# Kernel tuning notes

Measured on AMD Instinct MI355X. Metric: run time of the kernel, lower is better.

Reference implementation:

```python
import jax, jax.numpy as jnp
import numpy as np

B, F, D = 4096, 39, 16          # batch, num_field, embedding_size
V = 1000000                     # num_feat (vocab)
H1, H2 = 128, 128               # cin_layer_sizes
INPUT_DIM = F * D               # 624
FC_DIM = H1 // 2 + H2           # 192 (split_half)
DEEP = [400, 400]
BN_EPS = 1e-5


def setup_inputs() -> dict:
    key = jax.random.key(0)
    ks = jax.random.split(key, 16)
    xav = lambda k, shp: jax.random.normal(k, shp, jnp.float32) * np.sqrt(2.0 / (shp[0] + shp[-1]))
    return {
        "feat_index": jax.random.randint(ks[0], (B, F), 0, V),
        "feat_value": jax.random.uniform(ks[1], (B, F), jnp.float32),
        "emb_table": xav(ks[2], (V, D)),
        "linear_w": xav(ks[3], (INPUT_DIM, 1)),
        "linear_b": jnp.zeros((1,), jnp.float32),
        "conv_w1": xav(ks[4], (H1, F, F)),          # (out, h_prev, m) == conv1d 1x1 weight reshaped
        "conv_b1": jnp.zeros((H1,), jnp.float32),
        "conv_w2": xav(ks[5], (H2, H1 // 2, F)),
        "conv_b2": jnp.zeros((H2,), jnp.float32),
        "deep_w1": xav(ks[6], (INPUT_DIM, DEEP[0])),
        "deep_b1": jnp.zeros((DEEP[0],), jnp.float32),
        "bn_g1": jnp.ones((DEEP[0],), jnp.float32),
        "bn_b1": jnp.zeros((DEEP[0],), jnp.float32),
        "deep_w2": xav(ks[7], (DEEP[0], DEEP[1])),
        "deep_b2": jnp.zeros((DEEP[1],), jnp.float32),
        "bn_g2": jnp.ones((DEEP[1],), jnp.float32),
        "bn_b2": jnpp if False else jnp.zeros((DEEP[1],), jnp.float32),
        "out_w": xav(ks[8], (1 + FC_DIM + DEEP[1], 1)),
        "out_b": jnp.zeros((1,), jnp.float32),
    }


def _bn(x, g, b):
    # torch BatchNorm1d in training mode: biased batch variance
    m = x.mean(axis=0)
    v = x.var(axis=0)
    return g * (x - m) * jax.lax.rsqrt(v + BN_EPS) + b


def reference(feat_index, feat_value, emb_table, linear_w, linear_b,
              conv_w1, conv_b1, conv_w2, conv_b2,
              deep_w1, deep_b1, bn_g1, bn_b1,
              deep_w2, deep_b2, bn_g2, bn_b2,
              out_w, out_b):
    e = emb_table[feat_index]                      # [B, F, D]
    flat = e.reshape(e.shape[0], -1)               # [B, F*D]
    linear_part = flat @ linear_w + linear_b       # [B, 1]

    # CIN: fused outer-product + 1x1 conv (x_k[b,o,d] = sum_{h,m} W[o,h,m] x_prev[b,h,d] x0[b,m,d])
    x0 = e
    h1 = jax.nn.relu(jnp.einsum('bhd,bmd,ohm->bod', x0, x0, conv_w1) + conv_b1[None, :, None])
    nxt, hi1 = jnp.split(h1, 2, axis=1)            # split_half
    h2 = jax.nn.relu(jnp.einsum('bhd,bmd,ohm->bod', nxt, x0, conv_w2) + conv_b2[None, :, None])
    res = jnp.concatenate([hi1, h2], axis=1).sum(axis=2)   # [B, FC_DIM]

    # Deep tower (dropout off / deterministic)
    y = jax.nn.relu(_bn(flat @ deep_w1 + deep_b1, bn_g1, bn_b1))
    y = jax.nn.relu(_bn(y @ deep_w2 + deep_b2, bn_g2, bn_b2))

    cat = jnp.concatenate([linear_part, res, y], axis=1)   # [B, 593]
    return cat @ out_w + out_b
```

## Files before the change

kernel.cpp:

```cpp
#include <hip/hip_runtime.h>

#define BATCH   4096
#define NF      39
#define ED      16
#define IN_DIM  624
#define DW      400
#define BN_EPS  1e-5f
#define NK16    156
#define AK1     640
#define NKS1    20
#define NKS2    13
#define WCOL    416

typedef __attribute__((ext_vector_type(8))) short short8;
typedef __attribute__((ext_vector_type(16))) float f32x16;
typedef __attribute__((ext_vector_type(4))) float f32x4;
typedef __attribute__((ext_vector_type(2))) float f32x2;
typedef unsigned short u16;

__device__ inline unsigned pack_hi2(float a, float b) {
  return __builtin_amdgcn_perm(__float_as_uint(b), __float_as_uint(a), 0x07060302u);
}
__device__ inline unsigned bf16_rne(float f) {
  unsigned u = __float_as_uint(f);
  u += 0x7fff + ((u >> 16) & 1);
  return u >> 16;
}
__device__ inline float bf2f(u16 v) { return __uint_as_float((unsigned)v << 16); }

#define CIN_E (NK16 * 128 * 16)
#define D1_E  (NKS1 * WCOL * 32)
#define D2_E  (NKS2 * WCOL * 32)
#define PREP_E (CIN_E + D1_E + D2_E + 1600)
#define PREP_B ((PREP_E + 255) / 256)
#define GATH_B (BATCH / 4)

__global__ __launch_bounds__(256) void k_gp(const int* __restrict__ idx,
    const float* __restrict__ emb, const float* __restrict__ lw,
    const float* __restrict__ lb, const float* __restrict__ w1,
    const float* __restrict__ w2, const float* __restrict__ dw1,
    const float* __restrict__ dw2, u16* __restrict__ flatb,
    float* __restrict__ lp, u16* __restrict__ wp1, u16* __restrict__ wp2,
    u16* __restrict__ wpd1, u16* __restrict__ wpd2, float* __restrict__ gstat) {
  int t = threadIdx.x;
  if (blockIdx.x < GATH_B) {
    int lane = t & 63;
    int b = blockIdx.x * 4 + (t >> 6);
    int sj = (lane < NF) ? idx[b * NF + lane] : 0;
    float acc = 0.f;
#pragma unroll
    for (int i = 0; i < 10; i++) {
      int e = lane + i * 64;
      if (e < IN_DIM) {
        int f = e >> 4;
        int row = __shfl(sj, f);
        float v = emb[(size_t)row * ED + (e & 15)];
        flatb[(size_t)b * AK1 + e] = (u16)bf16_rne(v);
        acc = fmaf(v, lw[e], acc);
      } else {
        flatb[(size_t)b * AK1 + e] = 0;
      }
    }
#pragma unroll
    for (int k = 1; k < 64; k <<= 1) acc += __shfl_xor(acc, k);
    if (lane == 0) lp[b] = acc + lb[0];
  } else {
    int e = (blockIdx.x - GATH_B) * 256 + t;
    if (e < CIN_E) {
      int k16 = e >> 11, r = e & 2047, col = r >> 4, kk = r & 15;
      int k = k16 * 16 + kk, h = k & 63, m = k >> 6;
      float v1 = (h < NF) ? w1[(size_t)col * (NF * NF) + h * NF + m] : 0.f;
      float v2 = w2[(size_t)col * (64 * NF) + h * NF + m];
      wp1[e] = (u16)bf16_rne(v1);
      wp2[e] = (u16)bf16_rne(v2);
    } else if (e < CIN_E + D1_E) {
      int e2 = e - CIN_E;
      int ksg = e2 / (WCOL * 32), r = e2 - ksg * (WCOL * 32);
      int col = r >> 5, kk = r & 31;
      int k = ksg * 32 + kk;
      wpd1[e2] = (k < IN_DIM && col < DW) ? (u16)bf16_rne(dw1[(size_t)k * DW + col]) : 0;
    } else if (e < CIN_E + D1_E + D2_E) {
      int e2 = e - CIN_E - D1_E;
      int ksg = e2 / (WCOL * 32), r = e2 - ksg * (WCOL * 32);
      int col = r >> 5, kk = r & 31;
      int k = ksg * 32 + kk;
      wpd2[e2] = (k < DW && col < DW) ? (u16)bf16_rne(dw2[(size_t)k * DW + col]) : 0;
    } else if (e < PREP_E) {
      gstat[e - CIN_E - D1_E - D2_E] = 0.f;
    }
  }
}

template <bool LAY2>
__global__ __launch_bounds__(256, 2) void k_cin32(
    const u16* __restrict__ flatb, const u16* __restrict__ nxtg,
    const u16* __restrict__ wp, const float* __restrict__ bias,
    u16* __restrict__ nxt_out, float* __restrict__ res) {
  int t = threadIdx.x;
  int w = t >> 6, lane = t & 63;
  int col = lane & 31, khalf = lane >> 5;
  int si = (lane >> 4) & 1, d = lane & 15;
  int b0 = blockIdx.x * 8 + w * 2;
  int b = b0 + si;
  const u16* fb = flatb + (size_t)b * AK1;

  f32x2 sp[4][4];
  if (LAY2) {
#pragma unroll
    for (int s = 0; s < 4; s++) {
      uint4 v = *(const uint4*)(nxtg + (((size_t)b * 16 + d) * 64 + s * 16 + khalf * 8));
      unsigned uu[4] = {v.x, v.y, v.z, v.w};
#pragma unroll
      for (int w4 = 0; w4 < 4; w4++)
        sp[s][w4] = (f32x2){__uint_as_float(uu[w4] << 16),
                            __uint_as_float(uu[w4] & 0xffff0000u)};
    }
  } else {
#pragma unroll
    for (int s = 0; s < 4; s++)
#pragma unroll
      for (int w4 = 0; w4 < 4; w4++) {
        int h0 = s * 16 + khalf * 8 + 2 * w4;
        int h1 = h0 + 1;
        float f0 = (h0 < NF) ? bf2f(fb[h0 * 16 + d]) : 0.f;
        float f1 = (h1 < NF) ? bf2f(fb[h1 * 16 + d]) : 0.f;
        sp[s][w4] = (f32x2){f0, f1};
      }
  }

  f32x16 acc[4];
#pragma unroll
  for (int nt = 0; nt < 4; nt++)
#pragma unroll
    for (int r = 0; r < 16; r++) acc[nt][r] = 0.f;

  const u16* wbase = wp + (size_t)col * 16 + khalf * 8;
  short8 bfr[3][4];
#pragma unroll
  for (int nt = 0; nt < 4; nt++) {
    bfr[0][nt] = *(const short8*)(wbase + nt * 512);
    bfr[1][nt] = *(const short8*)(wbase + 2048 + nt * 512);
  }

  float xv = bf2f(fb[d]);
  float xvn;

  for (int mg = 0; mg < 13; mg++) {
#pragma unroll
    for (int j = 0; j < 12; j++) {
      int k16 = mg * 12 + j;
      if (j == 0 || j == 4 || j == 8) {
        int mn = mg * 3 + (j >> 2) + 1;
        xvn = bf2f(fb[mn * 16 + d]);
      }
      if (j < 10 || mg < 12) {
        const u16* wb = wbase + (size_t)(k16 + 2) * 2048;
#pragma unroll
        for (int nt = 0; nt < 4; nt++)
          bfr[(j + 2) % 3][nt] = *(const short8*)(wb + nt * 512);
      }
      int s = j & 3;
      union { unsigned u[4]; short8 v; } a;
      f32x2 xv2 = (f32x2){xv, xv};
#pragma unroll
      for (int w4 = 0; w4 < 4; w4++) {
        f32x2 p = sp[s][w4] * xv2;
        a.u[w4] = pack_hi2(p[0], p[1]);
      }
#pragma unroll
      for (int nt = 0; nt < 4; nt++)
        acc[nt] = __builtin_amdgcn_mfma_f32_32x32x16_bf16(
            a.v, bfr[j % 3][nt], acc[nt], 0, 0, 0);
      if (s == 3) xv = xvn;
    }
  }

#pragma unroll
  for (int nt = 0; nt < 4; nt++) {
    int o = nt * 32 + col;
    float bi = bias[o];
    if (!LAY2 && nt < 2) {
#pragma unroll
      for (int r = 0; r < 16; r++) {
        int si2 = r >> 3;
        int dd = (r & 3) + 8 * ((r >> 2) & 1) + 4 * khalf;
        float v = fmaxf(acc[nt][r] + bi, 0.f);
        nxt_out[((size_t)(b0 + si2) * 16 + dd) * 64 + o] = (u16)bf16_rne(v);
      }
    } else {
      float p0 = 0.f, p1 = 0.f;
#pragma unroll
      for (int r = 0; r < 8; r++)  p0 += fmaxf(acc[nt][r] + bi, 0.f);
#pragma unroll
      for (int r = 8; r < 16; r++) p1 += fmaxf(acc[nt][r] + bi, 0.f);
      p0 += __shfl_xor(p0, 32);
      p1 += __shfl_xor(p1, 32);
      if (khalf == 0) {
        int ri = LAY2 ? (64 + o) : (o - 64);
        res[(size_t)b0 * 192 + ri] = p0;
        res[(size_t)(b0 + 1) * 192 + ri] = p1;
      }
    }
  }
}

template <bool BN_A, int NKS, int KREAL, int AK>
__global__ __launch_bounds__(256) void k_gemm_mfma(
    const u16* __restrict__ Abf, const float* __restrict__ Af32,
    const u16* __restrict__ wp, const float* __restrict__ bias,
    const float* __restrict__ gsIn, const float* __restrict__ gs2In,
    const float* __restrict__ bng, const float* __restrict__ bnb,
    float* __restrict__ C, float* __restrict__ gs, float* __restrict__ gs2) {
  __shared__ float lsS[NKS * 32], lsH[NKS * 32];
  __shared__ float lred[64];
  int t = threadIdx.x;
  if (BN_A) {
    for (int c = t; c < NKS * 32; c += 256) {
      float sc = 0.f, sh = 0.f;
      if (c < DW) {
        float m = gsIn[c] * (1.f / BATCH);
        float var = gs2In[c] * (1.f / BATCH) - m * m;
        sc = bng[c] * rsqrtf(var + BN_EPS);
        sh = bnb[c] - m * sc;
      }
      lsS[c] = sc; lsH[c] = sh;
    }
  }
  if (t < 64) lred[t] = 0.f;
  __syncthreads();

  int w = t >> 6, lane = t & 63;
  int nl = lane & 15, q = lane >> 4;
  int row = blockIdx.x * 64 + w * 16 + nl;
  int c0 = blockIdx.y * 32;
  f32x4 acc[2];
  acc[0] = (f32x4){0.f, 0.f, 0.f, 0.f};
  acc[1] = (f32x4){0.f, 0.f, 0.f, 0.f};

  short8 araw[2]; f32x4 fraw0[2], fraw1[2]; short8 braw[2][2];
  auto loadA_raw = [&](int ksg, int buf) {
    int kb = ksg * 32 + q * 8;
    if (!BN_A) {
      araw[buf] = *(const short8*)(Abf + (size_t)row * AK + kb);
    } else {
      if (kb + 8 <= KREAL) {
        fraw0[buf] = *(const f32x4*)(Af32 + (size_t)row * KREAL + kb);
        fraw1[buf] = *(const f32x4*)(Af32 + (size_t)row * KREAL + kb + 4);
      } else {
        fraw0[buf] = (f32x4){0.f,0.f,0.f,0.f};
        fraw1[buf] = (f32x4){0.f,0.f,0.f,0.f};
      }
    }
    const u16* wb = wp + (size_t)ksg * (WCOL * 32) + (size_t)(c0 + nl) * 32 + q * 8;
    braw[buf][0] = *(const short8*)wb;
    braw[buf][1] = *(const short8*)(wb + 16 * 32);
  };
  auto cookA = [&](int ksg, int buf) -> short8 {
    if (!BN_A) return araw[buf];
    int kb = ksg * 32 + q * 8;
    f32x4 s0 = *(const f32x4*)&lsS[kb], h0 = *(const f32x4*)&lsH[kb];
    f32x4 s1 = *(const f32x4*)&lsS[kb + 4], h1 = *(const f32x4*)&lsH[kb + 4];
    union { unsigned u[4]; short8 s; } a;
    float v0 = fmaxf(fmaf(fraw0[buf][0], s0[0], h0[0]), 0.f);
    float v1 = fmaxf(fmaf(fraw0[buf][1], s0[1], h0[1]), 0.f);
    float v2 = fmaxf(fmaf(fraw0[buf][2], s0[2], h0[2]), 0.f);
    float v3 = fmaxf(fmaf(fraw0[buf][3], s0[3], h0[3]), 0.f);
    float v4 = fmaxf(fmaf(fraw1[buf][0], s1[0], h1[0]), 0.f);
    float v5 = fmaxf(fmaf(fraw1[buf][1], s1[1], h1[1]), 0.f);
    float v6 = fmaxf(fmaf(fraw1[buf][2], s1[2], h1[2]), 0.f);
    float v7 = fmaxf(fmaf(fraw1[buf][3], s1[3], h1[3]), 0.f);
    a.u[0] = bf16_rne(v0) | (bf16_rne(v1) << 16);
    a.u[1] = bf16_rne(v2) | (bf16_rne(v3) << 16);
    a.u[2] = bf16_rne(v4) | (bf16_rne(v5) << 16);
    a.u[3] = bf16_rne(v6) | (bf16_rne(v7) << 16);
    return a.s;
  };

  loadA_raw(0, 0);
#pragma unroll 4
  for (int ksg = 0; ksg < NKS; ksg++) {
    int cur = ksg & 1;
    if (ksg + 1 < NKS) loadA_raw(ksg + 1, cur ^ 1);
    short8 afr = cookA(ksg, cur);
    acc[0] = __builtin_amdgcn_mfma_f32_16x16x32_bf16(afr, braw[cur][0], acc[0], 0, 0, 0);
    acc[1] = __builtin_amdgcn_mfma_f32_16x16x32_bf16(afr, braw[cur][1], acc[1], 0, 0, 0);
  }

  int rbase = blockIdx.x * 64 + w * 16 + q * 4;
#pragma unroll
  for (int nt = 0; nt < 2; nt++) {
    int col = c0 + nt * 16 + nl;
    if (col < DW) {
      float bi = bias[col];
      float s = 0.f, s2 = 0.f;
#pragma unroll
      for (int r = 0; r < 4; r++) {
        float v = acc[nt][r] + bi;
        C[(size_t)(rbase + r) * DW + col] = v;
        s += v; s2 = fmaf(v, v, s2);
      }
      s += __shfl_xor(s, 16); s2 += __shfl_xor(s2, 16);
      s += __shfl_xor(s, 32); s2 += __shfl_xor(s2, 32);
      if (q == 0) {
        atomicAdd(&lred[nt * 16 + nl], s);
        atomicAdd(&lred[32 + nt * 16 + nl], s2);
      }
    }
  }
  __syncthreads();
  if (t < 32) {
    int col = c0 + t;
    if (col < DW) atomicAdd(&gs[col], lred[t]);
  } else if (t < 64) {
    int col = c0 + t - 32;
    if (col < DW) atomicAdd(&gs2[col], lred[t]);
  }
}

__global__ __launch_bounds__(256) void k_final(const float* __restrict__ lp,
    const float* __restrict__ res, const float* __restrict__ y2,
    const float* __restrict__ gB, const float* __restrict__ gB2,
    const float* __restrict__ g2, const float* __restrict__ bb2,
    const float* __restrict__ ow, const float* __restrict__ ob,
    float* __restrict__ out) {
  __shared__ float lsS[DW], lsH[DW];
  int t = threadIdx.x;
  for (int c = t; c < DW; c += 256) {
    float m = gB[c] * (1.f / BATCH);
    float var = gB2[c] * (1.f / BATCH) - m * m;
    float sc = g2[c] * rsqrtf(var + BN_EPS);
    lsS[c] = sc;
    lsH[c] = bb2[c] - m * sc;
  }
  __syncthreads();
  int lane = t & 63, w = t >> 6;
  int b = blockIdx.x * 4 + w;
  float acc = 0.f;
  for (int j = lane; j < 593; j += 64) {
    float v;
    if (j == 0)       v = lp[b];
    else if (j < 193) v = res[(size_t)b * 192 + (j - 1)];
    else {
      int c = j - 193;
      v = fmaxf(fmaf(y2[(size_t)b * DW + c], lsS[c], lsH[c]), 0.f);
    }
    acc = fmaf(v, ow[j], acc);
  }
#pragma unroll
  for (int k = 1; k < 64; k <<= 1) acc += __shfl_xor(acc, k);
  if (lane == 0) out[b] = acc + ob[0];
}

extern "C" void kernel_launch(void* const* d_in, const int* in_sizes, int n_in,
                              void* d_out, int out_size, void* d_ws, size_t ws_size,
                              hipStream_t stream) {
  const int*   feat_index = (const int*)d_in[0];
  const float* emb = (const float*)d_in[2];
  const float* lw  = (const float*)d_in[3];
  const float* lb  = (const float*)d_in[4];
  const float* w1  = (const float*)d_in[5];
  const float* b1  = (const float*)d_in[6];
  const float* w2  = (const float*)d_in[7];
  const float* b2  = (const float*)d_in[8];
  const float* dw1 = (const float*)d_in[9];
  const float* db1 = (const float*)d_in[10];
  const float* g1  = (const float*)d_in[11];
  const float* bb1 = (const float*)d_in[12];
  const float* dw2 = (const float*)d_in[13];
  const float* db2 = (const float*)d_in[14];
  const float* g2  = (const float*)d_in[15];
  const float* bb2 = (const float*)d_in[16];
  const float* ow  = (const float*)d_in[17];
  const float* ob  = (const float*)d_in[18];

  float* ws   = (float*)d_ws;
  u16*  flatb = (u16*)ws;
  float* y1   = ws + 1310720;
  float* res  = ws + 2949120;
  float* lp   = ws + 3735552;
  float* gA   = ws + 3741248;
  float* gA2  = gA + 400;
  float* gB   = gA2 + 400;
  float* gB2  = gB + 400;
  u16*  nxtg  = (u16*)(ws + 3742848);
  float* y2   = ws + 3742848;
  u16*  wp1   = (u16*)(ws + 5840000);
  u16*  wp2   = (u16*)(ws + 5999744);
  u16*  wpd1  = (u16*)(ws + 6159488);
  u16*  wpd2  = (u16*)(ws + 6292608);
  float* out  = (float*)d_out;

  k_gp<<<GATH_B + PREP_B, 256, 0, stream>>>(feat_index, emb, lw, lb, w1, w2,
      dw1, dw2, flatb, lp, wp1, wp2, wpd1, wpd2, gA);
  k_cin32<false><<<512, 256, 0, stream>>>(flatb, nullptr, wp1, b1, nxtg, res);
  k_cin32<true><<<512, 256, 0, stream>>>(flatb, nxtg, wp2, b2, nullptr, res);
  k_gemm_mfma<false, NKS1, IN_DIM, AK1><<<dim3(BATCH / 64, 13), 256, 0, stream>>>(
      flatb, nullptr, wpd1, db1, nullptr, nullptr, nullptr, nullptr, y1, gA, gA2);
  k_gemm_mfma<true, NKS2, DW, 0><<<dim3(BATCH / 64, 13), 256, 0, stream>>>(
      nullptr, y1, wpd2, db2, gA, gA2, g1, bb1, y2, gB, gB2);
  k_final<<<BATCH / 4, 256, 0, stream>>>(lp, res, y2, gB, gB2, g2, bb2, ow, ob, out);
}
```

Measured before the change: 269.4 us.

## Split CIN output channels across blocks and stage weights through LDS double buffer

```diff
diff --git a/kernel.cpp b/kernel.cpp
--- a/kernel.cpp
+++ b/kernel.cpp
@@ -92,17 +92,23 @@
 }
 
 template <bool LAY2>
-__global__ __launch_bounds__(256, 2) void k_cin32(
+__global__ __launch_bounds__(256, 4) void k_cin32(
     const u16* __restrict__ flatb, const u16* __restrict__ nxtg,
     const u16* __restrict__ wp, const float* __restrict__ bias,
     u16* __restrict__ nxt_out, float* __restrict__ res) {
+  __shared__ u16 bsm[2][1024];
   int t = threadIdx.x;
   int w = t >> 6, lane = t & 63;
   int col = lane & 31, khalf = lane >> 5;
   int si = (lane >> 4) & 1, d = lane & 15;
-  int b0 = blockIdx.x * 8 + w * 2;
+  int bid = blockIdx.x;
+  int b0 = (bid >> 1) * 8 + w * 2;
+  int c0 = (bid & 1) * 64;
   int b = b0 + si;
   const u16* fb = flatb + (size_t)b * AK1;
+
+  const u16* gchunk = wp + (size_t)(c0 + ((t >> 6) & 1) * 32 + (t & 31)) * 16
+                         + ((t >> 5) & 1) * 8;
 
   f32x2 sp[4][4];
   if (LAY2) {
@@ -128,37 +134,36 @@
       }
   }
 
-  f32x16 acc[4];
-#pragma unroll
-  for (int nt = 0; nt < 4; nt++)
+  f32x16 acc[2];
+#pragma unroll
+  for (int nt = 0; nt < 2; nt++)
 #pragma unroll
     for (int r = 0; r < 16; r++) acc[nt][r] = 0.f;
 
-  const u16* wbase = wp + (size_t)col * 16 + khalf * 8;
-  short8 bfr[3][4];
-#pragma unroll
-  for (int nt = 0; nt < 4; nt++) {
-    bfr[0][nt] = *(const short8*)(wbase + nt * 512);
-    bfr[1][nt] = *(const short8*)(wbase + 2048 + nt * 512);
-  }
+  uint4 stg;
+  if (t < 128) {
+    stg = *(const uint4*)gchunk;
+    *(uint4*)&bsm[0][(size_t)t * 8] = stg;
+  }
+  __syncthreads();
+  if (t < 128) stg = *(const uint4*)(gchunk + 2048);
 
   float xv = bf2f(fb[d]);
   float xvn;
+  int rdoff0 = khalf * 256 + col * 8;
+  int rdoff1 = 512 + khalf * 256 + col * 8;
 
   for (int mg = 0; mg < 13; mg++) {
 #pragma unroll
     for (int j = 0; j < 12; j++) {
       int k16 = mg * 12 + j;
+      int cur = k16 & 1;
       if (j == 0 || j == 4 || j == 8) {
         int mn = mg * 3 + (j >> 2) + 1;
         xvn = bf2f(fb[mn * 16 + d]);
       }
-      if (j < 10 || mg < 12) {
-        const u16* wb = wbase + (size_t)(k16 + 2) * 2048;
-#pragma unroll
-        for (int nt = 0; nt < 4; nt++)
-          bfr[(j + 2) % 3][nt] = *(const short8*)(wb + nt * 512);
-      }
+      short8 bfr0 = *(const short8*)&bsm[cur][rdoff0];
+      short8 bfr1 = *(const short8*)&bsm[cur][rdoff1];
       int s = j & 3;
       union { unsigned u[4]; short8 v; } a;
       f32x2 xv2 = (f32x2){xv, xv};
@@ -167,19 +172,23 @@
         f32x2 p = sp[s][w4] * xv2;
         a.u[w4] = pack_hi2(p[0], p[1]);
       }
-#pragma unroll
-      for (int nt = 0; nt < 4; nt++)
-        acc[nt] = __builtin_amdgcn_mfma_f32_32x32x16_bf16(
-            a.v, bfr[j % 3][nt], acc[nt], 0, 0, 0);
+      acc[0] = __builtin_amdgcn_mfma_f32_32x32x16_bf16(a.v, bfr0, acc[0], 0, 0, 0);
+      acc[1] = __builtin_amdgcn_mfma_f32_32x32x16_bf16(a.v, bfr1, acc[1], 0, 0, 0);
+      if (k16 + 1 < NK16 && t < 128) {
+        *(uint4*)&bsm[cur ^ 1][(size_t)t * 8] = stg;
+        if (k16 + 2 < NK16)
+          stg = *(const uint4*)(gchunk + (size_t)(k16 + 2) * 2048);
+      }
       if (s == 3) xv = xvn;
-    }
-  }
-
-#pragma unroll
-  for (int nt = 0; nt < 4; nt++) {
-    int o = nt * 32 + col;
+      __syncthreads();
+    }
+  }
+
+#pragma unroll
+  for (int nt = 0; nt < 2; nt++) {
+    int o = c0 + nt * 32 + col;
     float bi = bias[o];
-    if (!LAY2 && nt < 2) {
+    if (!LAY2 && c0 == 0) {
 #pragma unroll
       for (int r = 0; r < 16; r++) {
         int si2 = r >> 3;
@@ -392,8 +401,8 @@
 
   k_gp<<<GATH_B + PREP_B, 256, 0, stream>>>(feat_index, emb, lw, lb, w1, w2,
       dw1, dw2, flatb, lp, wp1, wp2, wpd1, wpd2, gA);
-  k_cin32<false><<<512, 256, 0, stream>>>(flatb, nullptr, wp1, b1, nxtg, res);
-  k_cin32<true><<<512, 256, 0, stream>>>(flatb, nxtg, wp2, b2, nullptr, res);
+  k_cin32<false><<<1024, 256, 0, stream>>>(flatb, nullptr, wp1, b1, nxtg, res);
+  k_cin32<true><<<1024, 256, 0, stream>>>(flatb, nxtg, wp2, b2, nullptr, res);
   k_gemm_mfma<false, NKS1, IN_DIM, AK1><<<dim3(BATCH / 64, 13), 256, 0, stream>>>(
       flatb, nullptr, wpd1, db1, nullptr, nullptr, nullptr, nullptr, y1, gA, gA2);
   k_gemm_mfma<true, NKS2, DW, 0><<<dim3(BATCH / 64, 13), 256, 0, stream>>>(
```

Result: no change. 273.3 us (+1.4%).
